# Performance work log

Measured on AMD Instinct MI355X. Metric: run time of the kernel, lower is better.

Reference implementation:

```python
import jax, jax.numpy as jnp
import numpy as np

POOL = 7
STRIDE = 16.0


def setup_inputs() -> dict:
    key = jax.random.key(0)
    k1, k2, k3, k4, k5 = jax.random.split(key, 5)
    image = jax.random.normal(k1, (1, 128, 128, 512), dtype=jnp.float32)
    N = 1000
    # RoIs in input-image pixel coords: (x_center, y_center, w, h)
    w = jax.random.uniform(k2, (N,), minval=32.0, maxval=480.0)
    h = jax.random.uniform(k3, (N,), minval=32.0, maxval=480.0)
    x0 = jax.random.uniform(k4, (N,), minval=0.0, maxval=1500.0)
    y0 = jax.random.uniform(k5, (N,), minval=0.0, maxval=1500.0)
    RoI = jnp.stack([x0 + w / 2, y0 + h / 2, w, h], axis=1).astype(jnp.float32)
    return {"image": image, "RoI_inImage": RoI}


def _axis_coords(start, size, pool, limit):
    """Half-pixel bilinear sample coords for resizing a [size]-long crop
    starting at `start` to `pool` samples (matches tf.image.resize bilinear).
    Returns (i0, i1, frac) each [N, pool]."""
    grid = (jnp.arange(pool, dtype=jnp.float32) + 0.5) / pool  # [pool]
    s = grid[None, :] * size[:, None] - 0.5                    # crop-relative
    s = jnp.clip(s, 0.0, size[:, None] - 1.0)
    f0 = jnp.floor(s)
    frac = s - f0
    f1 = jnp.minimum(f0 + 1.0, size[:, None] - 1.0)
    i0 = jnp.clip(start[:, None] + f0, 0, limit - 1).astype(jnp.int32)
    i1 = jnp.clip(start[:, None] + f1, 0, limit - 1).astype(jnp.int32)
    return i0, i1, frac


def _roi_pool(image, RoI):
    H, W = image.shape[1], image.shape[2]
    feat = image[0]  # [H, W, C]
    x, y, w, h = RoI[:, 0], RoI[:, 1], RoI[:, 2], RoI[:, 3]
    # integer crop bounds on the stride-16 feature map (non-differentiable)
    r = jax.lax.stop_gradient(jnp.round((x - w / 2) / STRIDE))   # col start
    c = jax.lax.stop_gradient(jnp.round((y - h / 2) / STRIDE))   # row start
    wq = jax.lax.stop_gradient(jnp.maximum(jnp.round(w / STRIDE), 1.0))
    hq = jax.lax.stop_gradient(jnp.maximum(jnp.round(h / STRIDE), 1.0))
    iy0, iy1, ly = _axis_coords(c, hq, POOL, H)  # rows   [N, P]
    ix0, ix1, lx = _axis_coords(r, wq, POOL, W)  # cols   [N, P]
    # gather 4 corners: [N, P, P, C]
    g = lambda iy, ix: feat[iy[:, :, None], ix[:, None, :]]
    ly_ = ly[:, :, None, None]
    lx_ = lx[:, None, :, None]
    out = ((1 - ly_) * (1 - lx_) * g(iy0, ix0)
           + (1 - ly_) * lx_ * g(iy0, ix1)
           + ly_ * (1 - lx_) * g(iy1, ix0)
           + ly_ * lx_ * g(iy1, ix1))
    N = RoI.shape[0]
    return out.reshape(1, N, POOL, POOL, feat.shape[-1])


def reference(image, RoI_inImage):
    return _roi_pool(image, RoI_inImage)
```

## Files before the change

kernel.cpp:

```cpp
#include <hip/hip_runtime.h>

#define POOL    7
#define RSTRIDE 16.0f
#define IMG_H   128
#define IMG_W   128
#define IMG_C   512
#define C4      (IMG_C / 4)

template <bool SWIZZLE>
__global__ __launch_bounds__(128)
void RoiPoolingLayer_22462678958491_kernel(const float* __restrict__ image,
                                           const float* __restrict__ roi,
                                           float* __restrict__ out, int N)
{
    int n, py;
    if (SWIZZLE) {
        const int per   = N >> 3;
        const int xcd   = blockIdx.x & 7;
        const int local = blockIdx.x >> 3;
        const int q     = local / POOL;
        n  = xcd * per + q;
        py = local - q * POOL;
    } else {
        n  = blockIdx.x / POOL;
        py = blockIdx.x - n * POOL;
    }

    const float x = roi[n * 4 + 0];
    const float y = roi[n * 4 + 1];
    const float w = roi[n * 4 + 2];
    const float h = roi[n * 4 + 3];

    const float r  = rintf((x - 0.5f * w) / RSTRIDE);
    const float c  = rintf((y - 0.5f * h) / RSTRIDE);
    const float wq = fmaxf(rintf(w / RSTRIDE), 1.0f);
    const float hq = fmaxf(rintf(h / RSTRIDE), 1.0f);

    float sy = (((float)py + 0.5f) / (float)POOL) * hq - 0.5f;
    sy = fminf(fmaxf(sy, 0.0f), hq - 1.0f);
    const float fy0 = floorf(sy);
    const float ly  = sy - fy0;
    const float fy1 = fminf(fy0 + 1.0f, hq - 1.0f);
    const int iy0 = (int)fminf(fmaxf(c + fy0, 0.0f), (float)(IMG_H - 1));
    const int iy1 = (int)fminf(fmaxf(c + fy1, 0.0f), (float)(IMG_H - 1));

    const int t = threadIdx.x;
    const float4* row0 = (const float4*)(image + (size_t)iy0 * IMG_W * IMG_C) + t;
    const float4* row1 = (const float4*)(image + (size_t)iy1 * IMG_W * IMG_C) + t;
    float4* po = (float4*)(out + ((size_t)n * (POOL * POOL) + (size_t)py * POOL) * IMG_C) + t;

#pragma unroll
    for (int px = 0; px < POOL; ++px) {
        float sx = (((float)px + 0.5f) / (float)POOL) * wq - 0.5f;
        sx = fminf(fmaxf(sx, 0.0f), wq - 1.0f);
        const float fx0 = floorf(sx);
        const float lx  = sx - fx0;
        const float fx1 = fminf(fx0 + 1.0f, wq - 1.0f);
        const int ix0 = (int)fminf(fmaxf(r + fx0, 0.0f), (float)(IMG_W - 1));
        const int ix1 = (int)fminf(fmaxf(r + fx1, 0.0f), (float)(IMG_W - 1));

        const float w00 = (1.0f - ly) * (1.0f - lx);
        const float w01 = (1.0f - ly) * lx;
        const float w10 = ly * (1.0f - lx);
        const float w11 = ly * lx;

        const float4 a  = row0[ix0 * C4];
        const float4 bb = row0[ix1 * C4];
        const float4 cc = row1[ix0 * C4];
        const float4 dd = row1[ix1 * C4];

        float4 o;
        o.x = w00 * a.x + w01 * bb.x + w10 * cc.x + w11 * dd.x;
        o.y = w00 * a.y + w01 * bb.y + w10 * cc.y + w11 * dd.y;
        o.z = w00 * a.z + w01 * bb.z + w10 * cc.z + w11 * dd.z;
        o.w = w00 * a.w + w01 * bb.w + w10 * cc.w + w11 * dd.w;
        po[px * C4] = o;
    }
}

extern "C" void kernel_launch(void* const* d_in, const int* in_sizes, int n_in,
                              void* d_out, int out_size, void* d_ws, size_t ws_size,
                              hipStream_t stream)
{
    const float* image = (const float*)d_in[0];
    const float* roi   = (const float*)d_in[1];
    float*       out   = (float*)d_out;

    const int N = in_sizes[1] / 4;
    const int blocks = N * POOL;

    if ((N & 7) == 0) {
        RoiPoolingLayer_22462678958491_kernel<true><<<blocks, 128, 0, stream>>>(image, roi, out, N);
    } else {
        RoiPoolingLayer_22462678958491_kernel<false><<<blocks, 128, 0, stream>>>(image, roi, out, N);
    }
}
```

Measured before the change: 150.1 us.

## Bin RoIs spatially per XCD for L2 locality and use nontemporal stores

Adds a single-block counting-sort kernel that buckets RoIs into 64 spatial bins by center, bit-interleaving the bin coordinates so each XCD's contiguous slice of the ordering covers a compact image region. The pooling kernel looks up its RoI through this ordering, aiming for better L2 reuse of image rows within each XCD. Output writes become nontemporal stores so they do not evict image data from cache. The cost is an extra serial launch and an indirection load. The bin uses only the RoI center rather than its extent, so large RoIs still span many bins.

```diff
diff --git a/kernel.cpp b/kernel.cpp
--- a/kernel.cpp
+++ b/kernel.cpp
@@ -6,21 +6,51 @@
 #define IMG_W   128
 #define IMG_C   512
 #define C4      (IMG_C / 4)
+#define NBINS   64
 
-template <bool SWIZZLE>
+typedef float f4v __attribute__((ext_vector_type(4)));
+
+__device__ __forceinline__ int roi_bin(const float* __restrict__ roi, int i) {
+    const float x = roi[i * 4 + 0];
+    const float y = roi[i * 4 + 1];
+    const int cx = (int)fminf(fmaxf(x * (1.0f / RSTRIDE), 0.0f), 127.0f);
+    const int cy = (int)fminf(fmaxf(y * (1.0f / RSTRIDE), 0.0f), 127.0f);
+    const int bx = cx >> 4, by = cy >> 4;
+    return (by & 1) | ((bx & 1) << 1) | ((by & 2) << 1) |
+           ((bx & 2) << 2) | ((by & 4) << 2) | ((bx & 4) << 3);
+}
+
+__global__ __launch_bounds__(256)
+void roi_sort_kernel(const float* __restrict__ roi, int N, int* __restrict__ order)
+{
+    __shared__ int cnt[NBINS], off[NBINS];
+    const int t = threadIdx.x;
+    if (t < NBINS) cnt[t] = 0;
+    __syncthreads();
+    for (int i = t; i < N; i += 256) atomicAdd(&cnt[roi_bin(roi, i)], 1);
+    __syncthreads();
+    if (t == 0) { int s = 0; for (int b = 0; b < NBINS; ++b) { off[b] = s; s += cnt[b]; } }
+    __syncthreads();
+    for (int i = t; i < N; i += 256) {
+        const int p = atomicAdd(&off[roi_bin(roi, i)], 1);
+        order[p] = i;
+    }
+}
+
+template <bool SORT>
 __global__ __launch_bounds__(128)
-void RoiPoolingLayer_22462678958491_kernel(const float* __restrict__ image,
-                                           const float* __restrict__ roi,
-                                           float* __restrict__ out, int N)
+void roi_pool_kernel(const float* __restrict__ image,
+                     const float* __restrict__ roi,
+                     float* __restrict__ out, int N,
+                     const int* __restrict__ order)
 {
     int n, py;
-    if (SWIZZLE) {
-        const int per   = N >> 3;
-        const int xcd   = blockIdx.x & 7;
-        const int local = blockIdx.x >> 3;
-        const int q     = local / POOL;
-        n  = xcd * per + q;
-        py = local - q * POOL;
+    if (SORT) {
+        const int xcd = blockIdx.x & 7;
+        const int j   = blockIdx.x >> 3;
+        const int q   = j / POOL;
+        py = j - q * POOL;
+        n  = order[xcd * (N >> 3) + q];
     } else {
         n  = blockIdx.x / POOL;
         py = blockIdx.x - n * POOL;
@@ -45,9 +75,9 @@
     const int iy1 = (int)fminf(fmaxf(c + fy1, 0.0f), (float)(IMG_H - 1));
 
     const int t = threadIdx.x;
-    const float4* row0 = (const float4*)(image + (size_t)iy0 * IMG_W * IMG_C) + t;
-    const float4* row1 = (const float4*)(image + (size_t)iy1 * IMG_W * IMG_C) + t;
-    float4* po = (float4*)(out + ((size_t)n * (POOL * POOL) + (size_t)py * POOL) * IMG_C) + t;
+    const f4v* row0 = (const f4v*)(image + (size_t)iy0 * IMG_W * IMG_C) + t;
+    const f4v* row1 = (const f4v*)(image + (size_t)iy1 * IMG_W * IMG_C) + t;
+    f4v* po = (f4v*)(out + ((size_t)n * (POOL * POOL) + (size_t)py * POOL) * IMG_C) + t;
 
 #pragma unroll
     for (int px = 0; px < POOL; ++px) {
@@ -64,17 +94,13 @@
         const float w10 = ly * (1.0f - lx);
         const float w11 = ly * lx;
 
-        const float4 a  = row0[ix0 * C4];
-        const float4 bb = row0[ix1 * C4];
-        const float4 cc = row1[ix0 * C4];
-        const float4 dd = row1[ix1 * C4];
+        const f4v a  = row0[ix0 * C4];
+        const f4v bb = row0[ix1 * C4];
+        const f4v cc = row1[ix0 * C4];
+        const f4v dd = row1[ix1 * C4];
 
-        float4 o;
-        o.x = w00 * a.x + w01 * bb.x + w10 * cc.x + w11 * dd.x;
-        o.y = w00 * a.y + w01 * bb.y + w10 * cc.y + w11 * dd.y;
-        o.z = w00 * a.z + w01 * bb.z + w10 * cc.z + w11 * dd.z;
-        o.w = w00 * a.w + w01 * bb.w + w10 * cc.w + w11 * dd.w;
-        po[px * C4] = o;
+        const f4v o = w00 * a + w01 * bb + w10 * cc + w11 * dd;
+        __builtin_nontemporal_store(o, po + px * C4);
     }
 }
 
@@ -88,10 +114,13 @@
 
     const int N = in_sizes[1] / 4;
     const int blocks = N * POOL;
+    int* order = (int*)d_ws;
 
-    if ((N & 7) == 0) {
-        RoiPoolingLayer_22462678958491_kernel<true><<<blocks, 128, 0, stream>>>(image, roi, out, N);
+    const bool sortable = ((N & 7) == 0) && ws_size >= (size_t)N * sizeof(int);
+    if (sortable) {
+        roi_sort_kernel<<<1, 256, 0, stream>>>(roi, N, order);
+        roi_pool_kernel<true><<<blocks, 128, 0, stream>>>(image, roi, out, N, order);
     } else {
-        RoiPoolingLayer_22462678958491_kernel<false><<<blocks, 128, 0, stream>>>(image, roi, out, N);
+        roi_pool_kernel<false><<<blocks, 128, 0, stream>>>(image, roi, out, N, order);
     }
 }
```

Measured after the change: 157.1 us. +4.7%, slower.
